# Kernel tuning notes

Hardware: AMD Instinct MI355X
Metric: run time of the kernel (lower is better)

The kernel has to match this reference:

```python
import jax, jax.numpy as jnp
import numpy as np

THINK_STEPS = 15
MAX_ANSWER_SZ = 30


def setup_inputs() -> dict:
    key = jax.random.key(0)
    ks = jax.random.split(key, 6)
    V, H, B, SQ = 95, 2048, 256, 162
    s = 1.0 / np.sqrt(H)
    x = jax.random.randint(ks[0], (B, SQ), 0, V, dtype=jnp.int64)
    W_ih = jax.random.uniform(ks[1], (4 * H, V), jnp.float32, -s, s)
    W_hh = jax.random.uniform(ks[2], (4 * H, H), jnp.float32, -s, s)
    b_ih = jax.random.uniform(ks[3], (4 * H,), jnp.float32, -s, s)
    b_hh = jax.random.uniform(ks[4], (4 * H,), jnp.float32, -s, s)
    W_proj = jax.random.uniform(ks[5], (V, H), jnp.float32, -s, s)
    return {"x": x, "W_ih": W_ih, "W_hh": W_hh, "b_ih": b_ih, "b_hh": b_hh, "W_proj": W_proj}


def reference(x, W_ih, W_hh, b_ih, b_hh, W_proj):
    V = W_ih.shape[1]
    H = W_hh.shape[1]
    B = x.shape[0]
    bias = b_ih + b_hh

    def cell(h, c, inp):
        # PyTorch gate order: i, f, g, o
        g = inp @ W_ih.T + h @ W_hh.T + bias  # (B, 4H)
        i, f, gg, o = jnp.split(g, 4, axis=-1)
        c_new = jax.nn.sigmoid(f) * c + jax.nn.sigmoid(i) * jnp.tanh(gg)
        h_new = jax.nn.sigmoid(o) * jnp.tanh(c_new)
        return h_new, c_new

    # Phase 1: consume one-hot question, seq-major (SQ, B, V)
    xs = jax.nn.one_hot(x.T, V, dtype=jnp.float32)
    h0 = jnp.zeros((B, H), jnp.float32)
    c0 = jnp.zeros((B, H), jnp.float32)

    def q_step(carry, xt):
        h, c = carry
        h, c = cell(h, c, xt)
        return (h, c), None

    (h, c), _ = jax.lax.scan(q_step, (h0, c0), xs)
    out_q = h  # `outputs` after question loop; NOT updated during thinking

    # Phase 2: 15 zero-input "thinking" steps (only state updated)
    zero_in = jnp.zeros((B, V), jnp.float32)

    def t_step(carry, _):
        h, c = carry
        h, c = cell(h, c, zero_in)
        return (h, c), None

    (h, c), _ = jax.lax.scan(t_step, (h, c), None, length=THINK_STEPS)

    def a_step(carry, _):
        out, h, c = carry
        logits = out @ W_proj.T  # (B, V)
        h_new, c_new = cell(h, c, logits)
        return (h_new, h_new, c_new), logits

    _, output_seq = jax.lax.scan(a_step, (out_q, h, c), None, length=MAX_ANSWER_SZ - 1)
    return output_seq.reshape(-1, V)  # ((A-1)*B, V)
```

## Files before the change

### kernel.cpp

```cpp
#include <hip/hip_runtime.h>


#define Hdim 2048
#define G4H  8192
#define Bsz  256
#define Vsz  95
#define SQL  162
#define TSTEPS 15
#define ASTEPS 29

typedef signed char i8;
typedef __attribute__((ext_vector_type(4))) int i32x4;

#define S_RANGE 0.0220970869121f
#define SWI (127.0f / S_RANGE)
#define SG  (S_RANGE / (127.0f * 127.0f))

__device__ __forceinline__ float sigm(float x) { return 1.0f / (1.0f + expf(-x)); }

__device__ __forceinline__ void quant2(float xl, i8& q1, i8& q2) {
  float a = rintf(xl);
  q1 = (i8)(int)a;
  q2 = (i8)(int)rintf((xl - a) * 128.0f);
}

#define LGKM_BAR                                            \
  asm volatile("s_waitcnt lgkmcnt(0)" ::: "memory");        \
  __builtin_amdgcn_s_barrier();

__global__ void k_split2(const float* __restrict__ w, i8* __restrict__ w1,
                         i8* __restrict__ w2) {
  for (long i = blockIdx.x * blockDim.x + threadIdx.x; i < (long)G4H * Hdim;
       i += (long)gridDim.x * blockDim.x) {
    int n = (int)(i >> 11), k = (int)(i & 2047);
    long r = (long)((n & 3) * Hdim + (n >> 2));
    float xl = w[r * Hdim + k] * SWI;
    i8 a, b;
    quant2(xl, a, b);
    w1[i] = a;
    w2[i] = b;
  }
}

__global__ void k_prep(const float* __restrict__ W_ih, const float* __restrict__ b_ih,
                       const float* __restrict__ b_hh, float* __restrict__ wihT2,
                       float* __restrict__ bias2, float* __restrict__ hf,
                       i8* __restrict__ h1, i8* __restrict__ h2) {
  int i = blockIdx.x * 256 + threadIdx.x;
  if (i < Vsz * G4H) {
    int v = i / G4H, n = i % G4H;
    int r = (n & 3) * Hdim + (n >> 2);
    wihT2[i] = W_ih[(long)r * Vsz + v];
  }
  if (i < G4H) {
    int r = (i & 3) * Hdim + (i >> 2);
    bias2[i] = b_ih[r] + b_hh[r];
  }
  if (i < Bsz * Hdim) {
    hf[i] = 0.f;
    h1[i] = 0;
    h2[i] = 0;
  }
}

__global__ __launch_bounds__(512) void k_step(
    const i8* __restrict__ a1p, const i8* __restrict__ a2p,
    const i8* __restrict__ b1p, const i8* __restrict__ b2p,
    const float* __restrict__ bias2, const float* __restrict__ wihT2,
    const float* __restrict__ lgp, const int* __restrict__ x, int tstep,
    int xstride, int mode, float* __restrict__ c, float* __restrict__ hf,
    i8* __restrict__ o1, i8* __restrict__ o2) {
  __shared__ __align__(16) i8 SM[49152];

  const int tid = threadIdx.x;
  const int wave = tid >> 6, lane = tid & 63;

  const int lin = blockIdx.x;
  const int lin2 = (lin & 7) * 32 + (lin >> 3);
  const int row0 = (lin2 & 1) * 128;
  const int col0 = (lin2 >> 1) * 64;

  const int wr = wave >> 1, wc = wave & 1;
  const int lr = lane & 15, lc = lane >> 4;

  const i8* gsrc[3];
  i8* wdst[3];
  {
    const int rr = lane >> 2;
    const int koff = ((lane & 3) ^ (rr & 3) ^ ((rr >> 2) & 3)) * 16;
#pragma unroll
    for (int j = 0; j < 3; ++j) {
      int cc = wave * 3 + j;
      const i8* base;
      long rg;
      if (cc < 8)       { base = a1p; rg = row0 + cc * 16; }
      else if (cc < 16) { base = a2p; rg = row0 + (cc - 8) * 16; }
      else if (cc < 20) { base = b1p; rg = col0 + (cc - 16) * 16; }
      else              { base = b2p; rg = col0 + (cc - 20) * 16; }
      gsrc[j] = base + (rg + rr) * (long)Hdim + koff;
      wdst[j] = SM + cc * 1024 + lane * 16;
    }
  }

  const int sl = (lc ^ (lr & 3) ^ ((lr >> 2) & 3)) * 16;
  int aoff[2], boff[2];
#pragma unroll
  for (int mf = 0; mf < 2; ++mf) aoff[mf] = (wr * 32 + mf * 16 + lr) * 64 + sl;
#pragma unroll
  for (int nf = 0; nf < 2; ++nf) boff[nf] = 16384 + (wc * 32 + nf * 16 + lr) * 64 + sl;

  i32x4 acc1[2][2] = {};
  i32x4 acc2[2][2] = {};
  const char* smb = (const char*)SM;
  i32x4 qA[3], qB[3], qC[3];

#define LOADQ(q, s)                                                   \
  { _Pragma("unroll") for (int j = 0; j < 3; ++j)                     \
        q[j] = *(const i32x4*)(gsrc[j] + (long)(s) * 64); }
#define WRITEQ(q, s)                                                  \
  { _Pragma("unroll") for (int j = 0; j < 3; ++j)                     \
        *(i32x4*)(wdst[j] + (((s) & 1) * 24576)) = q[j]; }

#define COMPUTE(kb)                                                             \
  {                                                                             \
    const char* sb = smb + ((kb) & 1) * 24576;                                  \
    i32x4 A10 = *(const i32x4*)(sb + aoff[0]);                                  \
    i32x4 A11 = *(const i32x4*)(sb + aoff[1]);                                  \
    i32x4 A20 = *(const i32x4*)(sb + 8192 + aoff[0]);                           \
    i32x4 A21 = *(const i32x4*)(sb + 8192 + aoff[1]);                           \
    i32x4 B10 = *(const i32x4*)(sb + boff[0]);                                  \
    i32x4 B11 = *(const i32x4*)(sb + boff[1]);                                  \
    i32x4 B20 = *(const i32x4*)(sb + 4096 + boff[0]);                           \
    i32x4 B21 = *(const i32x4*)(sb + 4096 + boff[1]);                           \
    __builtin_amdgcn_s_setprio(1);                                              \
    acc1[0][0] = __builtin_amdgcn_mfma_i32_16x16x64_i8(A10, B10, acc1[0][0], 0, 0, 0); \
    acc1[0][1] = __builtin_amdgcn_mfma_i32_16x16x64_i8(A10, B11, acc1[0][1], 0, 0, 0); \
    acc1[1][0] = __builtin_amdgcn_mfma_i32_16x16x64_i8(A11, B10, acc1[1][0], 0, 0, 0); \
    acc1[1][1] = __builtin_amdgcn_mfma_i32_16x16x64_i8(A11, B11, acc1[1][1], 0, 0, 0); \
    acc2[0][0] = __builtin_amdgcn_mfma_i32_16x16x64_i8(A10, B20, acc2[0][0], 0, 0, 0); \
    acc2[0][1] = __builtin_amdgcn_mfma_i32_16x16x64_i8(A10, B21, acc2[0][1], 0, 0, 0); \
    acc2[1][0] = __builtin_amdgcn_mfma_i32_16x16x64_i8(A11, B20, acc2[1][0], 0, 0, 0); \
    acc2[1][1] = __builtin_amdgcn_mfma_i32_16x16x64_i8(A11, B21, acc2[1][1], 0, 0, 0); \
    acc2[0][0] = __builtin_amdgcn_mfma_i32_16x16x64_i8(A20, B10, acc2[0][0], 0, 0, 0); \
    acc2[0][1] = __builtin_amdgcn_mfma_i32_16x16x64_i8(A20, B11, acc2[0][1], 0, 0, 0); \
    acc2[1][0] = __builtin_amdgcn_mfma_i32_16x16x64_i8(A21, B10, acc2[1][0], 0, 0, 0); \
    acc2[1][1] = __builtin_amdgcn_mfma_i32_16x16x64_i8(A21, B11, acc2[1][1], 0, 0, 0); \
    __builtin_amdgcn_s_setprio(0);                                              \
  }

  LOADQ(qA, 0); LOADQ(qB, 1); LOADQ(qC, 2);
  WRITEQ(qA, 0);
  LGKM_BAR;

  for (int t5 = 0; t5 < 5; ++t5) {
    const int kb0 = t5 * 6;
    if (kb0 + 3 <= 31) LOADQ(qA, kb0 + 3);
    WRITEQ(qB, kb0 + 1); COMPUTE(kb0); LGKM_BAR;
    if (kb0 + 4 <= 31) LOADQ(qB, kb0 + 4);
    WRITEQ(qC, kb0 + 2); COMPUTE(kb0 + 1); LGKM_BAR;
    if (kb0 + 5 <= 31) LOADQ(qC, kb0 + 5);
    WRITEQ(qA, kb0 + 3); COMPUTE(kb0 + 2); LGKM_BAR;
    if (kb0 + 6 <= 31) LOADQ(qA, kb0 + 6);
    WRITEQ(qB, kb0 + 4); COMPUTE(kb0 + 3); LGKM_BAR;
    if (kb0 + 7 <= 31) LOADQ(qB, kb0 + 7);
    WRITEQ(qC, kb0 + 5); COMPUTE(kb0 + 4); LGKM_BAR;
    if (kb0 + 8 <= 31) LOADQ(qC, kb0 + 8);
    WRITEQ(qA, kb0 + 6); COMPUTE(kb0 + 5); LGKM_BAR;
  }
  WRITEQ(qB, 31); COMPUTE(30); LGKM_BAR;
  COMPUTE(31);

  __syncthreads();
  float* gt = (float*)SM;
#pragma unroll
  for (int mf = 0; mf < 2; ++mf)
#pragma unroll
    for (int nf = 0; nf < 2; ++nf) {
      int col = wc * 32 + nf * 16 + lr;
#pragma unroll
      for (int i = 0; i < 4; ++i) {
        int row = wr * 32 + mf * 16 + lc * 4 + i;
        gt[row * 68 + col] =
            ((float)acc1[mf][nf][i] + (float)acc2[mf][nf][i] * 0.0078125f) * SG;
      }
    }
  __syncthreads();

  const int h16 = tid & 15;
  const int bl32 = tid >> 4;
  const int hh_g = (col0 >> 2) + h16;
  const float bi = bias2[col0 + 4 * h16 + 0];
  const float bf_ = bias2[col0 + 4 * h16 + 1];
  const float bg_ = bias2[col0 + 4 * h16 + 2];
  const float bo = bias2[col0 + 4 * h16 + 3];

  float ai[4] = {0, 0, 0, 0}, af[4] = {0, 0, 0, 0};
  float ag[4] = {0, 0, 0, 0}, ao[4] = {0, 0, 0, 0};
  if (mode == 2) {
    const float* wv0 = wihT2 + col0 + 4 * h16;
    for (int v = 0; v < Vsz; ++v) {
      const float* w4 = wv0 + (long)v * G4H;
      float w0 = w4[0], w1 = w4[1], w2 = w4[2], w3 = w4[3];
#pragma unroll
      for (int pr = 0; pr < 4; ++pr) {
        float l = lgp[(row0 + pr * 32 + bl32) * Vsz + v];
        ai[pr] += l * w0; af[pr] += l * w1; ag[pr] += l * w2; ao[pr] += l * w3;
      }
    }
  }

#pragma unroll
  for (int pr = 0; pr < 4; ++pr) {
    int brow = pr * 32 + bl32;
    int bg = row0 + brow;
    const float* gr = &gt[brow * 68 + 4 * h16];
    float xi = gr[0] + bi + ai[pr], xf = gr[1] + bf_ + af[pr];
    float xg = gr[2] + bg_ + ag[pr], xo = gr[3] + bo + ao[pr];
    if (mode == 1) {
      int tok = x[(bg * SQL + tstep) * xstride];
      const float* wv = wihT2 + (long)tok * G4H + col0 + 4 * h16;
      xi += wv[0]; xf += wv[1]; xg += wv[2]; xo += wv[3];
    }
    long ci = (long)bg * Hdim + hh_g;
    float cn = sigm(xf) * c[ci] + sigm(xi) * tanhf(xg);
    float hn = sigm(xo) * tanhf(cn);
    c[ci] = cn;
    hf[ci] = hn;
    i8 q1, q2;
    quant2(hn * 127.0f, q1, q2);
    o1[ci] = q1;
    o2[ci] = q2;
  }
#undef LOADQ
#undef WRITEQ
#undef COMPUTE
}

__global__ __launch_bounds__(256) void k_logits(const float* __restrict__ src,
                                                const float* __restrict__ Wp,
                                                float* __restrict__ lg,
                                                float* __restrict__ outp) {
  const int b = blockIdx.x, tid = threadIdx.x;
  const int wv = tid >> 6, ln = tid & 63;

  float4 hreg[8];
  const float4* srcv = (const float4*)(src + (long)b * Hdim);
#pragma unroll
  for (int i = 0; i < 8; ++i) hreg[i] = srcv[ln + 64 * i];

  for (int v = wv; v < Vsz; v += 4) {
    const float4* wrow = (const float4*)(Wp + (long)v * Hdim);
    float s = 0.f;
#pragma unroll
    for (int i = 0; i < 8; ++i) {
      float4 w = wrow[ln + 64 * i];
      s += w.x * hreg[i].x + w.y * hreg[i].y + w.z * hreg[i].z + w.w * hreg[i].w;
    }
#pragma unroll
    for (int off = 32; off; off >>= 1) s += __shfl_down(s, off);
    if (ln == 0) {
      lg[b * Vsz + v] = s;
      outp[b * Vsz + v] = s;
    }
  }
}

extern "C" void kernel_launch(void* const* d_in, const int* in_sizes, int n_in,
                              void* d_out, int out_size, void* d_ws, size_t ws_size,
                              hipStream_t stream) {
  const int* x = (const int*)d_in[0];
  const float* W_ih = (const float*)d_in[1];
  const float* W_hh = (const float*)d_in[2];
  const float* b_ih = (const float*)d_in[3];
  const float* b_hh = (const float*)d_in[4];
  const float* W_proj = (const float*)d_in[5];
  float* out = (float*)d_out;

  int xstride = (in_sizes[0] > Bsz * SQL) ? 2 : 1;

  i8* w1 = (i8*)d_ws;
  i8* w2 = w1 + (long)G4H * Hdim;
  float* wihT2 = (float*)(w2 + (long)G4H * Hdim);
  float* bias2 = wihT2 + (long)Vsz * G4H;
  float* hf = bias2 + G4H;
  float* c = hf + (long)Bsz * Hdim;
  float* outq = c + (long)Bsz * Hdim;
  float* lg = outq + (long)Bsz * Hdim;
  i8* h1A = (i8*)(lg + Bsz * Vsz);
  i8* h2A = h1A + (long)Bsz * Hdim;
  i8* h1B = h2A + (long)Bsz * Hdim;
  i8* h2B = h1B + (long)Bsz * Hdim;

  k_split2<<<4096, 256, 0, stream>>>(W_hh, w1, w2);
  k_prep<<<3040, 256, 0, stream>>>(W_ih, b_ih, b_hh, wihT2, bias2, hf, h1A, h2A);

  hipMemsetAsync(c, 0, (long)Bsz * Hdim * sizeof(float), stream);

  i8* i1[2] = {h1A, h1B};
  i8* i2[2] = {h2A, h2B};
  int pp = 0;

  for (int t = 0; t < SQL; ++t) {
    k_step<<<256, 512, 0, stream>>>(i1[pp], i2[pp], w1, w2, bias2, wihT2,
                                    nullptr, x, t, xstride, 1, c, hf,
                                    i1[pp ^ 1], i2[pp ^ 1]);
    pp ^= 1;
  }
  hipMemcpyAsync(outq, hf, (long)Bsz * Hdim * sizeof(float),
                 hipMemcpyDeviceToDevice, stream);

  for (int t = 0; t < TSTEPS; ++t) {
    k_step<<<256, 512, 0, stream>>>(i1[pp], i2[pp], w1, w2, bias2, wihT2,
                                    nullptr, nullptr, 0, 1, 0, c, hf,
                                    i1[pp ^ 1], i2[pp ^ 1]);
    pp ^= 1;
  }

  for (int s = 0; s < ASTEPS; ++s) {
    const float* src = (s == 0) ? outq : hf;
    k_logits<<<Bsz, 256, 0, stream>>>(src, W_proj, lg, out + (long)s * Bsz * Vsz);
    k_step<<<256, 512, 0, stream>>>(i1[pp], i2[pp], w1, w2, bias2, wihT2,
                                    lg, nullptr, 0, 1, 2, c, hf,
                                    i1[pp ^ 1], i2[pp ^ 1]);
    pp ^= 1;
  }
}
```

Before: 5.843 ms.

## Retile LSTM step to 64x64 blocks with 4 waves; batch four rows per logits block

The recurrent step kernel now uses 64-row by 64-column output tiles with 256 threads and 32KB of shared memory, launched as 512 blocks instead of 256 blocks of 512 threads. This spreads two smaller blocks per CU, which may improve latency hiding and scheduling. The cost is that each weight tile is reloaded by four row-blocks instead of two. The logits kernel now computes four batch rows per block, so each W_proj load is reused four times. That cuts it to 64 blocks and raises register pressure.

```diff
diff --git a/kernel.cpp b/kernel.cpp
--- a/kernel.cpp
+++ b/kernel.cpp
@@ -63,40 +63,40 @@
   }
 }
 
-__global__ __launch_bounds__(512) void k_step(
+__global__ __launch_bounds__(256) void k_step(
     const i8* __restrict__ a1p, const i8* __restrict__ a2p,
     const i8* __restrict__ b1p, const i8* __restrict__ b2p,
     const float* __restrict__ bias2, const float* __restrict__ wihT2,
     const float* __restrict__ lgp, const int* __restrict__ x, int tstep,
     int xstride, int mode, float* __restrict__ c, float* __restrict__ hf,
     i8* __restrict__ o1, i8* __restrict__ o2) {
-  __shared__ __align__(16) i8 SM[49152];
+  __shared__ __align__(16) i8 SM[32768];
 
   const int tid = threadIdx.x;
   const int wave = tid >> 6, lane = tid & 63;
 
   const int lin = blockIdx.x;
-  const int lin2 = (lin & 7) * 32 + (lin >> 3);
-  const int row0 = (lin2 & 1) * 128;
-  const int col0 = (lin2 >> 1) * 64;
+  const int lin2 = (lin & 7) * 64 + (lin >> 3);
+  const int row0 = (lin2 & 3) * 64;
+  const int col0 = (lin2 >> 2) * 64;
 
   const int wr = wave >> 1, wc = wave & 1;
   const int lr = lane & 15, lc = lane >> 4;
 
-  const i8* gsrc[3];
-  i8* wdst[3];
+  const i8* gsrc[4];
+  i8* wdst[4];
   {
     const int rr = lane >> 2;
     const int koff = ((lane & 3) ^ (rr & 3) ^ ((rr >> 2) & 3)) * 16;
 #pragma unroll
-    for (int j = 0; j < 3; ++j) {
-      int cc = wave * 3 + j;
+    for (int j = 0; j < 4; ++j) {
+      int cc = wave * 4 + j;
       const i8* base;
       long rg;
-      if (cc < 8)       { base = a1p; rg = row0 + cc * 16; }
-      else if (cc < 16) { base = a2p; rg = row0 + (cc - 8) * 16; }
-      else if (cc < 20) { base = b1p; rg = col0 + (cc - 16) * 16; }
-      else              { base = b2p; rg = col0 + (cc - 20) * 16; }
+      if (cc < 4)       { base = a1p; rg = row0 + cc * 16; }
+      else if (cc < 8)  { base = a2p; rg = row0 + (cc - 4) * 16; }
+      else if (cc < 12) { base = b1p; rg = col0 + (cc - 8) * 16; }
+      else              { base = b2p; rg = col0 + (cc - 12) * 16; }
       gsrc[j] = base + (rg + rr) * (long)Hdim + koff;
       wdst[j] = SM + cc * 1024 + lane * 16;
     }
@@ -107,27 +107,27 @@
 #pragma unroll
   for (int mf = 0; mf < 2; ++mf) aoff[mf] = (wr * 32 + mf * 16 + lr) * 64 + sl;
 #pragma unroll
-  for (int nf = 0; nf < 2; ++nf) boff[nf] = 16384 + (wc * 32 + nf * 16 + lr) * 64 + sl;
+  for (int nf = 0; nf < 2; ++nf) boff[nf] = 8192 + (wc * 32 + nf * 16 + lr) * 64 + sl;
 
   i32x4 acc1[2][2] = {};
   i32x4 acc2[2][2] = {};
   const char* smb = (const char*)SM;
-  i32x4 qA[3], qB[3], qC[3];
+  i32x4 qA[4], qB[4], qC[4];
 
 #define LOADQ(q, s)                                                   \
-  { _Pragma("unroll") for (int j = 0; j < 3; ++j)                     \
+  { _Pragma("unroll") for (int j = 0; j < 4; ++j)                     \
         q[j] = *(const i32x4*)(gsrc[j] + (long)(s) * 64); }
 #define WRITEQ(q, s)                                                  \
-  { _Pragma("unroll") for (int j = 0; j < 3; ++j)                     \
-        *(i32x4*)(wdst[j] + (((s) & 1) * 24576)) = q[j]; }
+  { _Pragma("unroll") for (int j = 0; j < 4; ++j)                     \
+        *(i32x4*)(wdst[j] + (((s) & 1) * 16384)) = q[j]; }
 
 #define COMPUTE(kb)                                                             \
   {                                                                             \
-    const char* sb = smb + ((kb) & 1) * 24576;                                  \
+    const char* sb = smb + ((kb) & 1) * 16384;                                  \
     i32x4 A10 = *(const i32x4*)(sb + aoff[0]);                                  \
     i32x4 A11 = *(const i32x4*)(sb + aoff[1]);                                  \
-    i32x4 A20 = *(const i32x4*)(sb + 8192 + aoff[0]);                           \
-    i32x4 A21 = *(const i32x4*)(sb + 8192 + aoff[1]);                           \
+    i32x4 A20 = *(const i32x4*)(sb + 4096 + aoff[0]);                           \
+    i32x4 A21 = *(const i32x4*)(sb + 4096 + aoff[1]);                           \
     i32x4 B10 = *(const i32x4*)(sb + boff[0]);                                  \
     i32x4 B11 = *(const i32x4*)(sb + boff[1]);                                  \
     i32x4 B20 = *(const i32x4*)(sb + 4096 + boff[0]);                           \
@@ -187,7 +187,7 @@
   __syncthreads();
 
   const int h16 = tid & 15;
-  const int bl32 = tid >> 4;
+  const int bl16 = tid >> 4;
   const int hh_g = (col0 >> 2) + h16;
   const float bi = bias2[col0 + 4 * h16 + 0];
   const float bf_ = bias2[col0 + 4 * h16 + 1];
@@ -203,7 +203,7 @@
       float w0 = w4[0], w1 = w4[1], w2 = w4[2], w3 = w4[3];
 #pragma unroll
       for (int pr = 0; pr < 4; ++pr) {
-        float l = lgp[(row0 + pr * 32 + bl32) * Vsz + v];
+        float l = lgp[(row0 + pr * 16 + bl16) * Vsz + v];
         ai[pr] += l * w0; af[pr] += l * w1; ag[pr] += l * w2; ao[pr] += l * w3;
       }
     }
@@ -211,7 +211,7 @@
 
 #pragma unroll
   for (int pr = 0; pr < 4; ++pr) {
-    int brow = pr * 32 + bl32;
+    int brow = pr * 16 + bl16;
     int bg = row0 + brow;
     const float* gr = &gt[brow * 68 + 4 * h16];
     float xi = gr[0] + bi + ai[pr], xf = gr[1] + bf_ + af[pr];
@@ -240,27 +240,44 @@
                                                 const float* __restrict__ Wp,
                                                 float* __restrict__ lg,
                                                 float* __restrict__ outp) {
-  const int b = blockIdx.x, tid = threadIdx.x;
+  const int b0 = blockIdx.x * 4, tid = threadIdx.x;
   const int wv = tid >> 6, ln = tid & 63;
 
-  float4 hreg[8];
-  const float4* srcv = (const float4*)(src + (long)b * Hdim);
-#pragma unroll
-  for (int i = 0; i < 8; ++i) hreg[i] = srcv[ln + 64 * i];
+  float4 hreg[4][8];
+#pragma unroll
+  for (int r = 0; r < 4; ++r) {
+    const float4* srcv = (const float4*)(src + (long)(b0 + r) * Hdim);
+#pragma unroll
+    for (int i = 0; i < 8; ++i) hreg[r][i] = srcv[ln + 64 * i];
+  }
 
   for (int v = wv; v < Vsz; v += 4) {
     const float4* wrow = (const float4*)(Wp + (long)v * Hdim);
-    float s = 0.f;
+    float s0 = 0.f, s1 = 0.f, s2 = 0.f, s3 = 0.f;
 #pragma unroll
     for (int i = 0; i < 8; ++i) {
       float4 w = wrow[ln + 64 * i];
-      s += w.x * hreg[i].x + w.y * hreg[i].y + w.z * hreg[i].z + w.w * hreg[i].w;
-    }
-#pragma unroll
-    for (int off = 32; off; off >>= 1) s += __shfl_down(s, off);
+      s0 += w.x * hreg[0][i].x + w.y * hreg[0][i].y + w.z * hreg[0][i].z + w.w * hreg[0][i].w;
+      s1 += w.x * hreg[1][i].x + w.y * hreg[1][i].y + w.z * hreg[1][i].z + w.w * hreg[1][i].w;
+      s2 += w.x * hreg[2][i].x + w.y * hreg[2][i].y + w.z * hreg[2][i].z + w.w * hreg[2][i].w;
+      s3 += w.x * hreg[3][i].x + w.y * hreg[3][i].y + w.z * hreg[3][i].z + w.w * hreg[3][i].w;
+    }
+#pragma unroll
+    for (int off = 32; off; off >>= 1) {
+      s0 += __shfl_down(s0, off);
+      s1 += __shfl_down(s1, off);
+      s2 += __shfl_down(s2, off);
+      s3 += __shfl_down(s3, off);
+    }
     if (ln == 0) {
-      lg[b * Vsz + v] = s;
-      outp[b * Vsz + v] = s;
+      lg[(b0 + 0) * Vsz + v] = s0;
+      lg[(b0 + 1) * Vsz + v] = s1;
+      lg[(b0 + 2) * Vsz + v] = s2;
+      lg[(b0 + 3) * Vsz + v] = s3;
+      outp[(b0 + 0) * Vsz + v] = s0;
+      outp[(b0 + 1) * Vsz + v] = s1;
+      outp[(b0 + 2) * Vsz + v] = s2;
+      outp[(b0 + 3) * Vsz + v] = s3;
     }
   }
 }
@@ -301,7 +318,7 @@
   int pp = 0;
 
   for (int t = 0; t < SQL; ++t) {
-    k_step<<<256, 512, 0, stream>>>(i1[pp], i2[pp], w1, w2, bias2, wihT2,
+    k_step<<<512, 256, 0, stream>>>(i1[pp], i2[pp], w1, w2, bias2, wihT2,
                                     nullptr, x, t, xstride, 1, c, hf,
                                     i1[pp ^ 1], i2[pp ^ 1]);
     pp ^= 1;
@@ -310,7 +327,7 @@
                  hipMemcpyDeviceToDevice, stream);
 
   for (int t = 0; t < TSTEPS; ++t) {
-    k_step<<<256, 512, 0, stream>>>(i1[pp], i2[pp], w1, w2, bias2, wihT2,
+    k_step<<<512, 256, 0, stream>>>(i1[pp], i2[pp], w1, w2, bias2, wihT2,
                                     nullptr, nullptr, 0, 1, 0, c, hf,
                                     i1[pp ^ 1], i2[pp ^ 1]);
     pp ^= 1;
@@ -318,8 +335,8 @@
 
   for (int s = 0; s < ASTEPS; ++s) {
     const float* src = (s == 0) ? outq : hf;
-    k_logits<<<Bsz, 256, 0, stream>>>(src, W_proj, lg, out + (long)s * Bsz * Vsz);
-    k_step<<<256, 512, 0, stream>>>(i1[pp], i2[pp], w1, w2, bias2, wihT2,
+    k_logits<<<64, 256, 0, stream>>>(src, W_proj, lg, out + (long)s * Bsz * Vsz);
+    k_step<<<512, 256, 0, stream>>>(i1[pp], i2[pp], w1, w2, bias2, wihT2,
                                     lg, nullptr, 0, 1, 2, c, hf,
                                     i1[pp ^ 1], i2[pp ^ 1]);
     pp ^= 1;
```

Result: slower. 5.973 ms (+2.2%).
